# Kernel tuning notes

Hardware: AMD Instinct MI355X
Metric: run time of the kernel (lower is better)

Reference implementation:

```python
import jax, jax.numpy as jnp
import numpy as np

EMBED_DIM = 128
NUM_HEADS = 4
WIN = (7, 7)
N = WIN[0] * WIN[1]  # 49
NW = 64              # windows per image
B = 128              # batch of images
SCALE = (EMBED_DIM // NUM_HEADS) ** -0.5


def _relative_position_index():
    coords = np.stack(np.meshgrid(np.arange(WIN[0]), np.arange(WIN[1]), indexing='ij'))
    cf = coords.reshape(2, -1)                       # [2, N]
    rel = cf[:, :, None] - cf[:, None, :]            # [2, N, N]
    rel = rel.transpose(1, 2, 0).astype(np.int64)    # [N, N, 2]
    rel[..., 0] += WIN[0] - 1
    rel[..., 0] *= 2 * WIN[1] - 1
    rel[..., 1] += WIN[1] - 1
    return rel.sum(-1).reshape(-1)                   # [N*N]


def setup_inputs() -> dict:
    key = jax.random.key(0)
    ks = jax.random.split(key, 6)
    C = EMBED_DIM
    x = jax.random.normal(ks[0], (NW * B, N, C), dtype=jnp.float32)
    mask = jnp.zeros((NW, N, N), dtype=jnp.float32)
    qkv_w = jax.random.normal(ks[1], (3 * C, C), dtype=jnp.float32) * (C ** -0.5)
    qkv_b = jnp.zeros((3 * C,), dtype=jnp.float32)
    proj_w = jax.random.normal(ks[2], (C, C), dtype=jnp.float32) * (C ** -0.5)
    proj_b = jnp.zeros((C,), dtype=jnp.float32)
    bias_table = jax.random.normal(ks[3], ((2 * WIN[0] - 1) * (2 * WIN[1] - 1), NUM_HEADS), dtype=jnp.float32) * 0.02
    rel_index = jnp.asarray(_relative_position_index(), dtype=jnp.int32)
    return {"x": x, "mask": mask, "qkv_w": qkv_w, "qkv_b": qkv_b,
            "proj_w": proj_w, "proj_b": proj_b, "bias_table": bias_table,
            "rel_index": rel_index}


def reference(x, mask, qkv_w, qkv_b, proj_w, proj_b, bias_table, rel_index):
    nwb, n, c = x.shape
    nh, ch = NUM_HEADS, c // NUM_HEADS
    qkv = x @ qkv_w.T + qkv_b                               # [nwb, n, 3c]
    qkv = qkv.reshape(nwb, n, 3, nh, ch)
    q, k, v = (jnp.moveaxis(qkv, (2, 3), (0, 2))[i] for i in range(3))  # each [nwb, nh, n, ch]
    attn = jnp.einsum('whik,whjk->whij', q * SCALE, k)      # [nwb, nh, n, n]
    # relative position bias: gather then reshape to [1, nh, n, n]
    bias = bias_table[rel_index].reshape(n, n, nh).transpose(2, 0, 1)[None]
    attn = attn + bias
    if mask is not None:
        nw = mask.shape[0]
        attn = attn.reshape(nwb // nw, nw, nh, n, n) + mask[None, :, None]
        attn = attn.reshape(nwb, nh, n, n)
    attn = jax.nn.softmax(attn, axis=-1)
    out = jnp.einsum('whij,whjd->whid', attn, v)            # [nwb, nh, n, ch]
    out = out.transpose(0, 2, 1, 3).reshape(nwb, n, c)
    return out @ proj_w.T + proj_b
```

## Files before the change

kernel.cpp:

```cpp
#include <hip/hip_runtime.h>

typedef __bf16 bf16x8 __attribute__((ext_vector_type(8)));
typedef __bf16 bf16x4 __attribute__((ext_vector_type(4)));
typedef float  f32x4  __attribute__((ext_vector_type(4)));

#define NTOK  49
#define CDIM  128
#define QK_SCALE 0.17677669529663687f

#define WQKV_OFF  0
#define WPROJ_OFF 98304
#define BIASF_OFF 131072

__device__ __forceinline__ int swz(int row, int col) {
    return (col & ~63) | ((((col >> 3) ^ row) & 7) << 3) | (col & 7);
}

__global__ void prep_kernel(const float* __restrict__ qkv_w,
                            const float* __restrict__ proj_w,
                            const float* __restrict__ bias_table,
                            const int*   __restrict__ rel_index,
                            __bf16* __restrict__ wqkv,
                            __bf16* __restrict__ wproj,
                            float*  __restrict__ biasf) {
    int t = blockIdx.x * 256 + threadIdx.x;
    if (t < 384 * 128) wqkv[t]  = (__bf16)qkv_w[t];
    if (t < 128 * 128) wproj[t] = (__bf16)proj_w[t];
    if (t < 4 * 2401) {
        int h = t / 2401, ij = t % 2401;
        biasf[t] = bias_table[rel_index[ij] * 4 + h];
    }
}

__launch_bounds__(256, 3)
__global__ void winattn_kernel(const float* __restrict__ x,
                               const float* __restrict__ mask,
                               const float* __restrict__ qkv_b,
                               const float* __restrict__ proj_b,
                               const __bf16* __restrict__ wqkv,
                               const __bf16* __restrict__ wproj,
                               const float* __restrict__ biasf,
                               float* __restrict__ out) {
    __shared__ __bf16 lds_a[64 * 128];
    __shared__ __bf16 lds_b[64 * 256];

    const int tid  = threadIdx.x;
    const int w    = blockIdx.x;
    const int wave = tid >> 6;
    const int lane = tid & 63;
    const int quad = lane >> 4;
    const int l16  = lane & 15;

    {
        int row = tid >> 2;
        int c0  = (tid & 3) * 32;
        __align__(16) __bf16 tmp[32];
        if (row < NTOK) {
            const float4* src = (const float4*)(x + ((size_t)w * NTOK + row) * CDIM + c0);
            #pragma unroll
            for (int i = 0; i < 8; ++i) {
                float4 f = src[i];
                tmp[i*4+0] = (__bf16)f.x; tmp[i*4+1] = (__bf16)f.y;
                tmp[i*4+2] = (__bf16)f.z; tmp[i*4+3] = (__bf16)f.w;
            }
        } else {
            #pragma unroll
            for (int i = 0; i < 32; ++i) tmp[i] = (__bf16)0.0f;
        }
        #pragma unroll
        for (int i = 0; i < 4; ++i)
            *(bf16x8*)&lds_a[row * 128 + swz(row, c0 + i*8)] = *(bf16x8*)&tmp[i*8];
    }
    __syncthreads();

    bf16x4 vreg[2][4];
    #pragma unroll
    for (int half = 0; half < 2; ++half) {
        const int oq = (half*4 + wave) * 16 + l16;
        const int ok = 128 + (wave*2 + half) * 16 + l16;
        const int ov = 256 + (half*4 + wave) * 16 + l16;
        f32x4 acc[3][4];
        #pragma unroll
        for (int a = 0; a < 3; ++a)
            #pragma unroll
            for (int b = 0; b < 4; ++b) acc[a][b] = (f32x4){0.f,0.f,0.f,0.f};

        #pragma unroll
        for (int kt = 0; kt < 4; ++kt) {
            bf16x8 a4[4];
            #pragma unroll
            for (int mt = 0; mt < 4; ++mt) {
                int rr = mt*16 + l16;
                a4[mt] = *(bf16x8*)&lds_a[rr * 128 + swz(rr, kt*32 + quad*8)];
            }
            bf16x8 bq = *(const bf16x8*)(wqkv + (size_t)oq * CDIM + kt*32 + quad*8);
            bf16x8 bk = *(const bf16x8*)(wqkv + (size_t)ok * CDIM + kt*32 + quad*8);
            bf16x8 bv = *(const bf16x8*)(wqkv + (size_t)ov * CDIM + kt*32 + quad*8);
            #pragma unroll
            for (int mt = 0; mt < 4; ++mt) {
                acc[0][mt] = __builtin_amdgcn_mfma_f32_16x16x32_bf16(a4[mt], bq, acc[0][mt], 0, 0, 0);
                acc[1][mt] = __builtin_amdgcn_mfma_f32_16x16x32_bf16(a4[mt], bk, acc[1][mt], 0, 0, 0);
                acc[2][mt] = __builtin_amdgcn_mfma_f32_16x16x32_bf16(a4[mt], bv, acc[2][mt], 0, 0, 0);
            }
        }
        float bqb = qkv_b[oq], bkb = qkv_b[ok], bvb = qkv_b[ov];
        #pragma unroll
        for (int mt = 0; mt < 4; ++mt) {
            #pragma unroll
            for (int r = 0; r < 4; ++r) {
                int row = mt*16 + quad*4 + r;
                lds_b[row*256 + swz(row, oq)] = (__bf16)((acc[0][mt][r] + bqb) * QK_SCALE);
                lds_b[row*256 + swz(row, ok)] = (__bf16)(acc[1][mt][r] + bkb);
            }
            bf16x4 vv;
            #pragma unroll
            for (int r = 0; r < 4; ++r) vv[r] = (__bf16)(acc[2][mt][r] + bvb);
            vreg[half][mt] = vv;
        }
    }
    __syncthreads();

    #pragma unroll
    for (int half = 0; half < 2; ++half) {
        int vc = (half*4 + wave) * 16 + l16;
        #pragma unroll
        for (int mt = 0; mt < 4; ++mt) {
            int tok = mt*16 + quad*4;
            *(bf16x4*)&lds_a[vc * 64 + swz(vc, tok)] = vreg[half][mt];
        }
    }

    {
        const int h = wave;
        bf16x8 bk[4];
        #pragma unroll
        for (int nt = 0; nt < 4; ++nt) {
            int rr = nt*16 + l16;
            bk[nt] = *(bf16x8*)&lds_b[rr*256 + swz(rr, 128 + h*32 + quad*8)];
        }
        f32x4 s[4][4];
        #pragma unroll
        for (int mt = 0; mt < 4; ++mt) {
            int rr = mt*16 + l16;
            bf16x8 aq = *(bf16x8*)&lds_b[rr*256 + swz(rr, h*32 + quad*8)];
            #pragma unroll
            for (int nt = 0; nt < 4; ++nt) {
                f32x4 z = (f32x4){0.f,0.f,0.f,0.f};
                s[mt][nt] = __builtin_amdgcn_mfma_f32_16x16x32_bf16(aq, bk[nt], z, 0, 0, 0);
            }
        }

        const float* bh = biasf + h * 2401;
        const float* mh = mask + (size_t)(w & 63) * 2401;
        #pragma unroll
        for (int mt = 0; mt < 4; ++mt) {
            #pragma unroll
            for (int r = 0; r < 4; ++r) {
                int i = mt*16 + quad*4 + r;
                float v[4];
                #pragma unroll
                for (int nt = 0; nt < 4; ++nt) {
                    int j = nt*16 + l16;
                    float t = s[mt][nt][r];
                    if (j < NTOK) { if (i < NTOK) t += bh[i*49 + j] + mh[i*49 + j]; }
                    else t = -1e30f;
                    v[nt] = t;
                }
                float mx = fmaxf(fmaxf(v[0], v[1]), fmaxf(v[2], v[3]));
                mx = fmaxf(mx, __shfl_xor(mx, 1, 64));
                mx = fmaxf(mx, __shfl_xor(mx, 2, 64));
                mx = fmaxf(mx, __shfl_xor(mx, 4, 64));
                mx = fmaxf(mx, __shfl_xor(mx, 8, 64));
                float e[4], sum = 0.f;
                #pragma unroll
                for (int nt = 0; nt < 4; ++nt) { e[nt] = __expf(v[nt] - mx); sum += e[nt]; }
                sum += __shfl_xor(sum, 1, 64);
                sum += __shfl_xor(sum, 2, 64);
                sum += __shfl_xor(sum, 4, 64);
                sum += __shfl_xor(sum, 8, 64);
                float inv = 1.0f / sum;
                #pragma unroll
                for (int nt = 0; nt < 4; ++nt) s[mt][nt][r] = e[nt] * inv;
            }
        }
        __syncthreads();
        #pragma unroll
        for (int mt = 0; mt < 4; ++mt)
            #pragma unroll
            for (int r = 0; r < 4; ++r) {
                int prow = (h << 6) + mt*16 + quad*4 + r;
                #pragma unroll
                for (int nt = 0; nt < 4; ++nt)
                    lds_b[prow*64 + swz(prow, nt*16 + l16)] = (__bf16)s[mt][nt][r];
            }
    }
    __syncthreads();

    {
        const int h = wave;
        bf16x8 bv[2][2];
        #pragma unroll
        for (int nv = 0; nv < 2; ++nv)
            #pragma unroll
            for (int kt = 0; kt < 2; ++kt) {
                int vr = h*32 + nv*16 + l16;
                bv[nv][kt] = *(bf16x8*)&lds_a[vr*64 + swz(vr, kt*32 + quad*8)];
            }
        bf16x8 ap[4][2];
        #pragma unroll
        for (int mt = 0; mt < 4; ++mt)
            #pragma unroll
            for (int kt = 0; kt < 2; ++kt) {
                int pr = (h << 6) + mt*16 + l16;
                ap[mt][kt] = *(bf16x8*)&lds_b[pr*64 + swz(pr, kt*32 + quad*8)];
            }
        __syncthreads();

        f32x4 oacc[4][2];
        #pragma unroll
        for (int a = 0; a < 4; ++a)
            #pragma unroll
            for (int b = 0; b < 2; ++b) oacc[a][b] = (f32x4){0.f,0.f,0.f,0.f};
        #pragma unroll
        for (int mt = 0; mt < 4; ++mt)
            #pragma unroll
            for (int kt = 0; kt < 2; ++kt)
                #pragma unroll
                for (int nv = 0; nv < 2; ++nv)
                    oacc[mt][nv] = __builtin_amdgcn_mfma_f32_16x16x32_bf16(
                        ap[mt][kt], bv[nv][kt], oacc[mt][nv], 0, 0, 0);

        #pragma unroll
        for (int mt = 0; mt < 4; ++mt)
            #pragma unroll
            for (int nv = 0; nv < 2; ++nv)
                #pragma unroll
                for (int r = 0; r < 4; ++r) {
                    int row = mt*16 + quad*4 + r;
                    lds_b[row*128 + swz(row, h*32 + nv*16 + l16)] = (__bf16)oacc[mt][nv][r];
                }
    }
    __syncthreads();

    #pragma unroll
    for (int ntl = 0; ntl < 2; ++ntl) {
        int o = (wave*2 + ntl) * 16 + l16;
        f32x4 acc[4];
        #pragma unroll
        for (int a = 0; a < 4; ++a) acc[a] = (f32x4){0.f,0.f,0.f,0.f};
        #pragma unroll
        for (int kt = 0; kt < 4; ++kt) {
            bf16x8 bf = *(const bf16x8*)(wproj + (size_t)o * CDIM + kt*32 + quad*8);
            #pragma unroll
            for (int mt = 0; mt < 4; ++mt) {
                int rr = mt*16 + l16;
                bf16x8 af = *(bf16x8*)&lds_b[rr*128 + swz(rr, kt*32 + quad*8)];
                acc[mt] = __builtin_amdgcn_mfma_f32_16x16x32_bf16(af, bf, acc[mt], 0, 0, 0);
            }
        }
        float pb = proj_b[o];
        #pragma unroll
        for (int mt = 0; mt < 4; ++mt)
            #pragma unroll
            for (int r = 0; r < 4; ++r) {
                int row = mt*16 + quad*4 + r;
                if (row < NTOK)
                    out[((size_t)w * NTOK + row) * CDIM + o] = acc[mt][r] + pb;
            }
    }
}

extern "C" void kernel_launch(void* const* d_in, const int* in_sizes, int n_in,
                              void* d_out, int out_size, void* d_ws, size_t ws_size,
                              hipStream_t stream) {
    const float* x          = (const float*)d_in[0];
    const float* mask       = (const float*)d_in[1];
    const float* qkv_w      = (const float*)d_in[2];
    const float* qkv_b      = (const float*)d_in[3];
    const float* proj_w     = (const float*)d_in[4];
    const float* proj_b     = (const float*)d_in[5];
    const float* bias_table = (const float*)d_in[6];
    const int*   rel_index  = (const int*)d_in[7];

    __bf16* wqkv  = (__bf16*)((char*)d_ws + WQKV_OFF);
    __bf16* wproj = (__bf16*)((char*)d_ws + WPROJ_OFF);
    float*  biasf = (float*)((char*)d_ws + BIASF_OFF);

    int nwb = in_sizes[0] / (NTOK * CDIM);

    prep_kernel<<<192, 256, 0, stream>>>(qkv_w, proj_w, bias_table, rel_index,
                                         wqkv, wproj, biasf);
    winattn_kernel<<<nwb, 256, 0, stream>>>(x, mask, qkv_b, proj_b,
                                            wqkv, wproj, biasf, (float*)d_out);
}
```

Baseline: 551.1 us.

## Transpose MFMA operand order, drop softmax max, pre-pad bf16 bias and mask

Swaps the A/B operands of the Q, K, S, PV and projection MFMAs so each lane owns whole rows. That turns the LDS stores and output writes into vectorised bf16x4/float4 accesses, and the row reductions into two cross-quad shuffles. The softmax drops max subtraction and uses exp2 with log2e folded into the Q scale, bias and mask. Normalisation is deferred to after PV, and one barrier is removed. Bias and mask are padded to 64x64 and converted to bf16 in the prep kernel, and the absent max subtraction risks overflow for large logits.

Result: no change. 543.7 us (-1.4%).

```diff
diff --git a/kernel.cpp b/kernel.cpp
--- a/kernel.cpp
+++ b/kernel.cpp
@@ -6,11 +6,13 @@
 
 #define NTOK  49
 #define CDIM  128
-#define QK_SCALE 0.17677669529663687f
+#define LOG2E 1.4426950408889634f
+#define QK2   (0.17677669529663687f * LOG2E)
 
 #define WQKV_OFF  0
 #define WPROJ_OFF 98304
-#define BIASF_OFF 131072
+#define BIASB_OFF 131072
+#define MASKB_OFF 163840
 
 __device__ __forceinline__ int swz(int row, int col) {
     return (col & ~63) | ((((col >> 3) ^ row) & 7) << 3) | (col & 7);
@@ -20,26 +22,52 @@
                             const float* __restrict__ proj_w,
                             const float* __restrict__ bias_table,
                             const int*   __restrict__ rel_index,
+                            const float* __restrict__ mask,
                             __bf16* __restrict__ wqkv,
                             __bf16* __restrict__ wproj,
-                            float*  __restrict__ biasf) {
+                            __bf16* __restrict__ biasb,
+                            __bf16* __restrict__ maskb) {
     int t = blockIdx.x * 256 + threadIdx.x;
     if (t < 384 * 128) wqkv[t]  = (__bf16)qkv_w[t];
     if (t < 128 * 128) wproj[t] = (__bf16)proj_w[t];
-    if (t < 4 * 2401) {
-        int h = t / 2401, ij = t % 2401;
-        biasf[t] = bias_table[rel_index[ij] * 4 + h];
+    if (t < 4096) {
+        int base = t * 4;
+        int h = base >> 12, i = (base >> 6) & 63, j0 = base & 63;
+        bf16x4 v;
+        #pragma unroll
+        for (int r = 0; r < 4; ++r) {
+            int j = j0 + r;
+            float f = 0.f;
+            if (i < NTOK && j < NTOK) f = bias_table[rel_index[i*49 + j] * 4 + h] * LOG2E;
+            v[r] = (__bf16)f;
+        }
+        *(bf16x4*)&biasb[base] = v;
+    }
+    {
+        int base = t * 4;
+        int wm = base >> 12, i = (base >> 6) & 63, j0 = base & 63;
+        bf16x4 v;
+        #pragma unroll
+        for (int r = 0; r < 4; ++r) {
+            int j = j0 + r;
+            float f;
+            if (j >= NTOK)      f = -1e30f;
+            else if (i < NTOK)  f = mask[wm*2401 + i*49 + j] * LOG2E;
+            else                f = 0.f;
+            v[r] = (__bf16)f;
+        }
+        *(bf16x4*)&maskb[base] = v;
     }
 }
 
 __launch_bounds__(256, 3)
 __global__ void winattn_kernel(const float* __restrict__ x,
-                               const float* __restrict__ mask,
                                const float* __restrict__ qkv_b,
                                const float* __restrict__ proj_b,
                                const __bf16* __restrict__ wqkv,
                                const __bf16* __restrict__ wproj,
-                               const float* __restrict__ biasf,
+                               const __bf16* __restrict__ biasb,
+                               const __bf16* __restrict__ maskb,
                                float* __restrict__ out) {
     __shared__ __bf16 lds_a[64 * 128];
     __shared__ __bf16 lds_b[64 * 256];
@@ -76,45 +104,49 @@
     bf16x4 vreg[2][4];
     #pragma unroll
     for (int half = 0; half < 2; ++half) {
-        const int oq = (half*4 + wave) * 16 + l16;
-        const int ok = 128 + (wave*2 + half) * 16 + l16;
-        const int ov = 256 + (half*4 + wave) * 16 + l16;
-        f32x4 acc[3][4];
-        #pragma unroll
-        for (int a = 0; a < 3; ++a)
-            #pragma unroll
-            for (int b = 0; b < 4; ++b) acc[a][b] = (f32x4){0.f,0.f,0.f,0.f};
-
+        const int tq = half*4 + wave;
+        const int tk = wave*2 + half;
+        const int tv = half*4 + wave;
+        f32x4 aq[4], ak[4], av[4];
+        #pragma unroll
+        for (int m = 0; m < 4; ++m) {
+            aq[m] = (f32x4){0.f,0.f,0.f,0.f};
+            ak[m] = (f32x4){0.f,0.f,0.f,0.f};
+            av[m] = (f32x4){0.f,0.f,0.f,0.f};
+        }
         #pragma unroll
         for (int kt = 0; kt < 4; ++kt) {
-            bf16x8 a4[4];
+            bf16x8 xf[4];
             #pragma unroll
             for (int mt = 0; mt < 4; ++mt) {
                 int rr = mt*16 + l16;
-                a4[mt] = *(bf16x8*)&lds_a[rr * 128 + swz(rr, kt*32 + quad*8)];
-            }
-            bf16x8 bq = *(const bf16x8*)(wqkv + (size_t)oq * CDIM + kt*32 + quad*8);
-            bf16x8 bk = *(const bf16x8*)(wqkv + (size_t)ok * CDIM + kt*32 + quad*8);
-            bf16x8 bv = *(const bf16x8*)(wqkv + (size_t)ov * CDIM + kt*32 + quad*8);
+                xf[mt] = *(bf16x8*)&lds_a[rr * 128 + swz(rr, kt*32 + quad*8)];
+            }
+            bf16x8 wq = *(const bf16x8*)(wqkv + (size_t)(      tq*16 + l16) * CDIM + kt*32 + quad*8);
+            bf16x8 wk = *(const bf16x8*)(wqkv + (size_t)(128 + tk*16 + l16) * CDIM + kt*32 + quad*8);
+            bf16x8 wv = *(const bf16x8*)(wqkv + (size_t)(256 + tv*16 + l16) * CDIM + kt*32 + quad*8);
             #pragma unroll
             for (int mt = 0; mt < 4; ++mt) {
-                acc[0][mt] = __builtin_amdgcn_mfma_f32_16x16x32_bf16(a4[mt], bq, acc[0][mt], 0, 0, 0);
-                acc[1][mt] = __builtin_amdgcn_mfma_f32_16x16x32_bf16(a4[mt], bk, acc[1][mt], 0, 0, 0);
-                acc[2][mt] = __builtin_amdgcn_mfma_f32_16x16x32_bf16(a4[mt], bv, acc[2][mt], 0, 0, 0);
-            }
-        }
-        float bqb = qkv_b[oq], bkb = qkv_b[ok], bvb = qkv_b[ov];
+                aq[mt] = __builtin_amdgcn_mfma_f32_16x16x32_bf16(wq, xf[mt], aq[mt], 0, 0, 0);
+                ak[mt] = __builtin_amdgcn_mfma_f32_16x16x32_bf16(wk, xf[mt], ak[mt], 0, 0, 0);
+                av[mt] = __builtin_amdgcn_mfma_f32_16x16x32_bf16(xf[mt], wv, av[mt], 0, 0, 0);
+            }
+        }
+        float4 bq4 = *(const float4*)&qkv_b[      tq*16 + quad*4];
+        float4 bk4 = *(const float4*)&qkv_b[128 + tk*16 + quad*4];
+        float  bv1 = qkv_b[256 + tv*16 + l16];
         #pragma unroll
         for (int mt = 0; mt < 4; ++mt) {
+            int row = mt*16 + l16;
+            bf16x4 qv, kv, vv;
             #pragma unroll
             for (int r = 0; r < 4; ++r) {
-                int row = mt*16 + quad*4 + r;
-                lds_b[row*256 + swz(row, oq)] = (__bf16)((acc[0][mt][r] + bqb) * QK_SCALE);
-                lds_b[row*256 + swz(row, ok)] = (__bf16)(acc[1][mt][r] + bkb);
-            }
-            bf16x4 vv;
-            #pragma unroll
-            for (int r = 0; r < 4; ++r) vv[r] = (__bf16)(acc[2][mt][r] + bvb);
+                qv[r] = (__bf16)((aq[mt][r] + ((const float*)&bq4)[r]) * QK2);
+                kv[r] = (__bf16)( ak[mt][r] + ((const float*)&bk4)[r]);
+                vv[r] = (__bf16)( av[mt][r] + bv1);
+            }
+            *(bf16x4*)&lds_b[row*256 + swz(row,       tq*16 + quad*4)] = qv;
+            *(bf16x4*)&lds_b[row*256 + swz(row, 128 + tk*16 + quad*4)] = kv;
             vreg[half][mt] = vv;
         }
     }
@@ -122,151 +154,139 @@
 
     #pragma unroll
     for (int half = 0; half < 2; ++half) {
-        int vc = (half*4 + wave) * 16 + l16;
-        #pragma unroll
-        for (int mt = 0; mt < 4; ++mt) {
-            int tok = mt*16 + quad*4;
-            *(bf16x4*)&lds_a[vc * 64 + swz(vc, tok)] = vreg[half][mt];
-        }
-    }
-
+        int vc = (half*4 + wave)*16 + l16;
+        #pragma unroll
+        for (int mt = 0; mt < 4; ++mt)
+            *(bf16x4*)&lds_a[vc * 64 + swz(vc, mt*16 + quad*4)] = vreg[half][mt];
+    }
+
+    const int h = wave;
+    float inv[4];
     {
-        const int h = wave;
-        bf16x8 bk[4];
-        #pragma unroll
-        for (int nt = 0; nt < 4; ++nt) {
-            int rr = nt*16 + l16;
-            bk[nt] = *(bf16x8*)&lds_b[rr*256 + swz(rr, 128 + h*32 + quad*8)];
-        }
-        f32x4 s[4][4];
-        #pragma unroll
-        for (int mt = 0; mt < 4; ++mt) {
-            int rr = mt*16 + l16;
-            bf16x8 aq = *(bf16x8*)&lds_b[rr*256 + swz(rr, h*32 + quad*8)];
-            #pragma unroll
-            for (int nt = 0; nt < 4; ++nt) {
+        bf16x8 kf[4], qf[4];
+        #pragma unroll
+        for (int t = 0; t < 4; ++t) {
+            int rr = t*16 + l16;
+            kf[t] = *(bf16x8*)&lds_b[rr*256 + swz(rr, 128 + h*32 + quad*8)];
+            qf[t] = *(bf16x8*)&lds_b[rr*256 + swz(rr,       h*32 + quad*8)];
+        }
+        __syncthreads();
+
+        f32x4 s2[4][4];
+        #pragma unroll
+        for (int mtq = 0; mtq < 4; ++mtq)
+            #pragma unroll
+            for (int ntk = 0; ntk < 4; ++ntk) {
                 f32x4 z = (f32x4){0.f,0.f,0.f,0.f};
-                s[mt][nt] = __builtin_amdgcn_mfma_f32_16x16x32_bf16(aq, bk[nt], z, 0, 0, 0);
-            }
-        }
-
-        const float* bh = biasf + h * 2401;
-        const float* mh = mask + (size_t)(w & 63) * 2401;
-        #pragma unroll
-        for (int mt = 0; mt < 4; ++mt) {
-            #pragma unroll
-            for (int r = 0; r < 4; ++r) {
-                int i = mt*16 + quad*4 + r;
-                float v[4];
+                s2[mtq][ntk] = __builtin_amdgcn_mfma_f32_16x16x32_bf16(kf[ntk], qf[mtq], z, 0, 0, 0);
+            }
+
+        const __bf16* bb = biasb + h * 4096;
+        const __bf16* mb = maskb + (size_t)(w & 63) * 4096;
+        #pragma unroll
+        for (int mtq = 0; mtq < 4; ++mtq) {
+            int i = mtq*16 + l16;
+            float e[4][4], sum = 0.f;
+            #pragma unroll
+            for (int ntk = 0; ntk < 4; ++ntk) {
+                int j0 = ntk*16 + quad*4;
+                bf16x4 b4 = *(const bf16x4*)&bb[i*64 + j0];
+                bf16x4 m4 = *(const bf16x4*)&mb[i*64 + j0];
                 #pragma unroll
-                for (int nt = 0; nt < 4; ++nt) {
-                    int j = nt*16 + l16;
-                    float t = s[mt][nt][r];
-                    if (j < NTOK) { if (i < NTOK) t += bh[i*49 + j] + mh[i*49 + j]; }
-                    else t = -1e30f;
-                    v[nt] = t;
+                for (int r = 0; r < 4; ++r) {
+                    float t = s2[mtq][ntk][r] + (float)b4[r] + (float)m4[r];
+                    e[ntk][r] = __builtin_amdgcn_exp2f(t);
+                    sum += e[ntk][r];
                 }
-                float mx = fmaxf(fmaxf(v[0], v[1]), fmaxf(v[2], v[3]));
-                mx = fmaxf(mx, __shfl_xor(mx, 1, 64));
-                mx = fmaxf(mx, __shfl_xor(mx, 2, 64));
-                mx = fmaxf(mx, __shfl_xor(mx, 4, 64));
-                mx = fmaxf(mx, __shfl_xor(mx, 8, 64));
-                float e[4], sum = 0.f;
+            }
+            sum += __shfl_xor(sum, 16, 64);
+            sum += __shfl_xor(sum, 32, 64);
+            inv[mtq] = __builtin_amdgcn_rcpf(sum);
+            #pragma unroll
+            for (int ntk = 0; ntk < 4; ++ntk) {
+                bf16x4 pv;
                 #pragma unroll
-                for (int nt = 0; nt < 4; ++nt) { e[nt] = __expf(v[nt] - mx); sum += e[nt]; }
-                sum += __shfl_xor(sum, 1, 64);
-                sum += __shfl_xor(sum, 2, 64);
-                sum += __shfl_xor(sum, 4, 64);
-                sum += __shfl_xor(sum, 8, 64);
-                float inv = 1.0f / sum;
-                #pragma unroll
-                for (int nt = 0; nt < 4; ++nt) s[mt][nt][r] = e[nt] * inv;
-            }
-        }
-        __syncthreads();
-        #pragma unroll
-        for (int mt = 0; mt < 4; ++mt)
-            #pragma unroll
-            for (int r = 0; r < 4; ++r) {
-                int prow = (h << 6) + mt*16 + quad*4 + r;
-                #pragma unroll
-                for (int nt = 0; nt < 4; ++nt)
-                    lds_b[prow*64 + swz(prow, nt*16 + l16)] = (__bf16)s[mt][nt][r];
-            }
-    }
-    __syncthreads();
+                for (int r = 0; r < 4; ++r) pv[r] = (__bf16)e[ntk][r];
+                *(bf16x4*)&lds_b[h*4096 + i*64 + swz(i, ntk*16 + quad*4)] = pv;
+            }
+        }
+    }
 
     {
-        const int h = wave;
-        bf16x8 bv[2][2];
+        bf16x8 vf[2][2];
         #pragma unroll
         for (int nv = 0; nv < 2; ++nv)
             #pragma unroll
             for (int kt = 0; kt < 2; ++kt) {
                 int vr = h*32 + nv*16 + l16;
-                bv[nv][kt] = *(bf16x8*)&lds_a[vr*64 + swz(vr, kt*32 + quad*8)];
-            }
-        bf16x8 ap[4][2];
-        #pragma unroll
-        for (int mt = 0; mt < 4; ++mt)
+                vf[nv][kt] = *(bf16x8*)&lds_a[vr*64 + swz(vr, kt*32 + quad*8)];
+            }
+        bf16x8 pf[4][2];
+        #pragma unroll
+        for (int mtq = 0; mtq < 4; ++mtq)
             #pragma unroll
             for (int kt = 0; kt < 2; ++kt) {
-                int pr = (h << 6) + mt*16 + l16;
-                ap[mt][kt] = *(bf16x8*)&lds_b[pr*64 + swz(pr, kt*32 + quad*8)];
+                int pr = mtq*16 + l16;
+                pf[mtq][kt] = *(bf16x8*)&lds_b[h*4096 + pr*64 + swz(pr, kt*32 + quad*8)];
             }
         __syncthreads();
 
-        f32x4 oacc[4][2];
-        #pragma unroll
-        for (int a = 0; a < 4; ++a)
-            #pragma unroll
-            for (int b = 0; b < 2; ++b) oacc[a][b] = (f32x4){0.f,0.f,0.f,0.f};
-        #pragma unroll
-        for (int mt = 0; mt < 4; ++mt)
+        f32x4 oacc[2][4];
+        #pragma unroll
+        for (int a = 0; a < 2; ++a)
+            #pragma unroll
+            for (int b = 0; b < 4; ++b) oacc[a][b] = (f32x4){0.f,0.f,0.f,0.f};
+        #pragma unroll
+        for (int mtq = 0; mtq < 4; ++mtq)
             #pragma unroll
             for (int kt = 0; kt < 2; ++kt)
                 #pragma unroll
                 for (int nv = 0; nv < 2; ++nv)
-                    oacc[mt][nv] = __builtin_amdgcn_mfma_f32_16x16x32_bf16(
-                        ap[mt][kt], bv[nv][kt], oacc[mt][nv], 0, 0, 0);
-
-        #pragma unroll
-        for (int mt = 0; mt < 4; ++mt)
-            #pragma unroll
-            for (int nv = 0; nv < 2; ++nv)
+                    oacc[nv][mtq] = __builtin_amdgcn_mfma_f32_16x16x32_bf16(
+                        vf[nv][kt], pf[mtq][kt], oacc[nv][mtq], 0, 0, 0);
+
+        #pragma unroll
+        for (int nv = 0; nv < 2; ++nv)
+            #pragma unroll
+            for (int mtq = 0; mtq < 4; ++mtq) {
+                int row = mtq*16 + l16;
+                bf16x4 ov;
                 #pragma unroll
-                for (int r = 0; r < 4; ++r) {
-                    int row = mt*16 + quad*4 + r;
-                    lds_b[row*128 + swz(row, h*32 + nv*16 + l16)] = (__bf16)oacc[mt][nv][r];
-                }
+                for (int r = 0; r < 4; ++r) ov[r] = (__bf16)(oacc[nv][mtq][r] * inv[mtq]);
+                *(bf16x4*)&lds_b[row*128 + swz(row, h*32 + nv*16 + quad*4)] = ov;
+            }
     }
     __syncthreads();
 
     #pragma unroll
     for (int ntl = 0; ntl < 2; ++ntl) {
-        int o = (wave*2 + ntl) * 16 + l16;
+        int oc = (wave*2 + ntl) * 16;
         f32x4 acc[4];
         #pragma unroll
         for (int a = 0; a < 4; ++a) acc[a] = (f32x4){0.f,0.f,0.f,0.f};
         #pragma unroll
         for (int kt = 0; kt < 4; ++kt) {
-            bf16x8 bf = *(const bf16x8*)(wproj + (size_t)o * CDIM + kt*32 + quad*8);
+            bf16x8 wf = *(const bf16x8*)(wproj + (size_t)(oc + l16) * CDIM + kt*32 + quad*8);
             #pragma unroll
             for (int mt = 0; mt < 4; ++mt) {
                 int rr = mt*16 + l16;
-                bf16x8 af = *(bf16x8*)&lds_b[rr*128 + swz(rr, kt*32 + quad*8)];
-                acc[mt] = __builtin_amdgcn_mfma_f32_16x16x32_bf16(af, bf, acc[mt], 0, 0, 0);
-            }
-        }
-        float pb = proj_b[o];
-        #pragma unroll
-        for (int mt = 0; mt < 4; ++mt)
-            #pragma unroll
-            for (int r = 0; r < 4; ++r) {
-                int row = mt*16 + quad*4 + r;
-                if (row < NTOK)
-                    out[((size_t)w * NTOK + row) * CDIM + o] = acc[mt][r] + pb;
-            }
+                bf16x8 of = *(bf16x8*)&lds_b[rr*128 + swz(rr, kt*32 + quad*8)];
+                acc[mt] = __builtin_amdgcn_mfma_f32_16x16x32_bf16(wf, of, acc[mt], 0, 0, 0);
+            }
+        }
+        float4 pb4 = *(const float4*)&proj_b[oc + quad*4];
+        #pragma unroll
+        for (int mt = 0; mt < 4; ++mt) {
+            int tok = mt*16 + l16;
+            if (tok < NTOK) {
+                float4 o4;
+                o4.x = acc[mt][0] + pb4.x;
+                o4.y = acc[mt][1] + pb4.y;
+                o4.z = acc[mt][2] + pb4.z;
+                o4.w = acc[mt][3] + pb4.w;
+                *(float4*)&out[((size_t)w * NTOK + tok) * CDIM + oc + quad*4] = o4;
+            }
+        }
     }
 }
 
@@ -284,12 +304,13 @@
 
     __bf16* wqkv  = (__bf16*)((char*)d_ws + WQKV_OFF);
     __bf16* wproj = (__bf16*)((char*)d_ws + WPROJ_OFF);
-    float*  biasf = (float*)((char*)d_ws + BIASF_OFF);
+    __bf16* biasb = (__bf16*)((char*)d_ws + BIASB_OFF);
+    __bf16* maskb = (__bf16*)((char*)d_ws + MASKB_OFF);
 
     int nwb = in_sizes[0] / (NTOK * CDIM);
 
-    prep_kernel<<<192, 256, 0, stream>>>(qkv_w, proj_w, bias_table, rel_index,
-                                         wqkv, wproj, biasf);
-    winattn_kernel<<<nwb, 256, 0, stream>>>(x, mask, qkv_b, proj_b,
-                                            wqkv, wproj, biasf, (float*)d_out);
+    prep_kernel<<<256, 256, 0, stream>>>(qkv_w, proj_w, bias_table, rel_index, mask,
+                                         wqkv, wproj, biasb, maskb);
+    winattn_kernel<<<nwb, 256, 0, stream>>>(x, qkv_b, proj_b,
+                                            wqkv, wproj, biasb, maskb, (float*)d_out);
 }
```
